# Kernel tuning notes

Hardware: AMD Instinct MI355X
Metric: run time of the kernel (lower is better)

Reference implementation:

```python
import jax, jax.numpy as jnp
import numpy as np


def _pool_matrix(in_size, out_size):
    # Reproduces TF adaptive window bounds: start = int(i*scale), end = ceil((i+1)*scale)
    scale = np.float32(in_size) / np.float32(out_size)
    idx = np.arange(out_size, dtype=np.float32)
    starts = (idx * scale).astype(np.int32)
    ends = np.ceil((idx + 1.0) * scale).astype(np.int32)
    M = np.zeros((out_size, in_size), dtype=np.float32)
    for i in range(out_size):  # loop over small static output size only
        M[i, starts[i]:ends[i]] = 1.0 / float(ends[i] - starts[i])
    return jnp.asarray(M)


def setup_inputs() -> dict:
    key = jax.random.key(0)
    x = jax.random.normal(key, (8, 224, 224, 256), dtype=jnp.float32)
    return {"x": x, "out_h": 7, "out_w": 7}


def reference(x, out_h, out_w):
    # x: [B, H, W, C] NHWC. Adaptive avg pool to [B, out_h, out_w, C].
    # Window means expressed as two small averaging matmuls (exactly equal to
    # the original slice+reduce_mean loops, applied rows-then-columns).
    Mh = _pool_matrix(x.shape[1], out_h)  # [out_h, H]
    Mw = _pool_matrix(x.shape[2], out_w)  # [out_w, W]
    xh = jnp.einsum('oh,bhwc->bowc', Mh, x)      # mean over row windows
    out = jnp.einsum('pw,bowc->bopc', Mw, xh)    # mean over col windows
    return out
```

## Files before the change

kernel.cpp:

```cpp
#include <hip/hip_runtime.h>


constexpr int B  = 8;
constexpr int H  = 224;
constexpr int W  = 224;
constexpr int C  = 256;
constexpr int OH = 7;
constexpr int OW = 7;
constexpr int WIN = 32;
constexpr int CHUNKS = 8;
constexpr int ROWS_PER_CHUNK = WIN / CHUNKS;
constexpr int G  = C / 4;
constexpr int OUT_ELEMS = B * OH * OW * C;
constexpr int NCHUNK_BLOCKS = B * OH * OW * CHUNKS;
constexpr size_t WS_NEEDED = (size_t)NCHUNK_BLOCKS * C * sizeof(float);

__global__ __launch_bounds__(256) void pool_partial_kernel(const float* __restrict__ x,
                                                           float* __restrict__ ws) {
    int bid   = blockIdx.x;
    int chunk = bid & (CHUNKS - 1);
    int t     = bid >> 3;
    int ow    = t % OW; t /= OW;
    int oh    = t % OH; t /= OH;
    int b     = t;

    int tid = threadIdx.x;
    int g   = tid & (G - 1);
    int r   = tid >> 6;

    int row  = oh * WIN + chunk * ROWS_PER_CHUNK + r;
    int col0 = ow * WIN;

    const float4* p = reinterpret_cast<const float4*>(
        x + (((size_t)b * H + row) * W + col0) * C) + g;

    float4 acc = make_float4(0.f, 0.f, 0.f, 0.f);
#pragma unroll
    for (int c = 0; c < WIN; ++c) {
        float4 v = p[(size_t)c * G];
        acc.x += v.x; acc.y += v.y; acc.z += v.z; acc.w += v.w;
    }

    __shared__ float4 lds[ROWS_PER_CHUNK][G];
    lds[r][g] = acc;
    __syncthreads();

    if (r == 0) {
        float4 a0 = lds[0][g];
        float4 a1 = lds[1][g];
        float4 a2 = lds[2][g];
        float4 a3 = lds[3][g];
        float4 s;
        s.x = a0.x + a1.x + a2.x + a3.x;
        s.y = a0.y + a1.y + a2.y + a3.y;
        s.z = a0.z + a1.z + a2.z + a3.z;
        s.w = a0.w + a1.w + a2.w + a3.w;
        reinterpret_cast<float4*>(ws)[(size_t)bid * G + g] = s;
    }
}

__global__ __launch_bounds__(256) void reduce_kernel(const float* __restrict__ ws,
                                                     float* __restrict__ out) {
    int i = blockIdx.x * 256 + threadIdx.x;
    if (i >= OUT_ELEMS) return;
    int o = i >> 8;
    int c = i & (C - 1);
    const float* p = ws + (size_t)(o * CHUNKS) * C + c;
    float s = 0.f;
#pragma unroll
    for (int k = 0; k < CHUNKS; ++k) s += p[(size_t)k * C];
    out[i] = s * (1.0f / (float)(WIN * WIN));
}

__global__ void zero_out_kernel(float* __restrict__ out, int n) {
    int i = blockIdx.x * blockDim.x + threadIdx.x;
    if (i < n) out[i] = 0.0f;
}

__global__ __launch_bounds__(256) void pool_atomic_kernel(const float* __restrict__ x,
                                                          float* __restrict__ out) {
    int bid   = blockIdx.x;
    int chunk = bid & (CHUNKS - 1);
    int t     = bid >> 3;
    int ow    = t % OW; t /= OW;
    int oh    = t % OH; t /= OH;
    int b     = t;

    int tid = threadIdx.x;
    int g   = tid & (G - 1);
    int r   = tid >> 6;

    int row  = oh * WIN + chunk * ROWS_PER_CHUNK + r;
    int col0 = ow * WIN;

    const float4* p = reinterpret_cast<const float4*>(
        x + (((size_t)b * H + row) * W + col0) * C) + g;

    float4 acc = make_float4(0.f, 0.f, 0.f, 0.f);
#pragma unroll
    for (int c = 0; c < WIN; ++c) {
        float4 v = p[(size_t)c * G];
        acc.x += v.x; acc.y += v.y; acc.z += v.z; acc.w += v.w;
    }

    __shared__ float4 lds[ROWS_PER_CHUNK][G];
    lds[r][g] = acc;
    __syncthreads();

    if (r == 0) {
        float4 a0 = lds[0][g];
        float4 a1 = lds[1][g];
        float4 a2 = lds[2][g];
        float4 a3 = lds[3][g];
        const float s = 1.0f / (float)(WIN * WIN);
        float* o = out + (size_t)(bid >> 3) * C + g * 4;
        atomicAdd(o + 0, (a0.x + a1.x + a2.x + a3.x) * s);
        atomicAdd(o + 1, (a0.y + a1.y + a2.y + a3.y) * s);
        atomicAdd(o + 2, (a0.z + a1.z + a2.z + a3.z) * s);
        atomicAdd(o + 3, (a0.w + a1.w + a2.w + a3.w) * s);
    }
}

extern "C" void kernel_launch(void* const* d_in, const int* in_sizes, int n_in,
                              void* d_out, int out_size, void* d_ws, size_t ws_size,
                              hipStream_t stream) {
    const float* x = (const float*)d_in[0];
    float* out = (float*)d_out;

    if (ws_size >= WS_NEEDED) {
        float* ws = (float*)d_ws;
        pool_partial_kernel<<<NCHUNK_BLOCKS, 256, 0, stream>>>(x, ws);
        reduce_kernel<<<(OUT_ELEMS + 255) / 256, 256, 0, stream>>>(ws, out);
    } else {
        zero_out_kernel<<<(OUT_ELEMS + 255) / 256, 256, 0, stream>>>(out, OUT_ELEMS);
        pool_atomic_kernel<<<NCHUNK_BLOCKS, 256, 0, stream>>>(x, out);
    }
}
```

Baseline: 78.25 us.

## Stream whole input rows per block and reduce row partials in second pass

```diff
diff --git a/kernel.cpp b/kernel.cpp
--- a/kernel.cpp
+++ b/kernel.cpp
@@ -8,12 +8,85 @@
 constexpr int OH = 7;
 constexpr int OW = 7;
 constexpr int WIN = 32;
+constexpr int G  = C / 4;
+constexpr int F4_PER_ROW = W * G;
+constexpr int ITERS = F4_PER_ROW / 256;
+constexpr int OUT_ELEMS = B * OH * OW * C;
+constexpr int NROWS = B * H;
+constexpr size_t WS_ROW_NEEDED = (size_t)NROWS * OW * C * sizeof(float);
+
+__global__ __launch_bounds__(256) void row_stream_kernel(const float* __restrict__ x,
+                                                         float* __restrict__ ws) {
+    const int rowid = blockIdx.x;
+    const int tid   = threadIdx.x;
+    const int c4    = tid & (G - 1);
+    const int col0  = tid >> 6;
+
+    const float4* p = reinterpret_cast<const float4*>(x) + (size_t)rowid * F4_PER_ROW + tid;
+
+    float4 acc[OW];
+#pragma unroll
+    for (int o = 0; o < OW; ++o) acc[o] = make_float4(0.f, 0.f, 0.f, 0.f);
+
+#pragma unroll
+    for (int m = 0; m < ITERS; ++m) {
+        float4 v = p[(size_t)m * 256];
+        const int o = m >> 3;
+        acc[o].x += v.x; acc[o].y += v.y; acc[o].z += v.z; acc[o].w += v.w;
+    }
+
+    __shared__ float4 lds[OW][2][G];
+
+    if (col0 >= 2) {
+#pragma unroll
+        for (int o = 0; o < OW; ++o) lds[o][col0 - 2][c4] = acc[o];
+    }
+    __syncthreads();
+    if (col0 < 2) {
+#pragma unroll
+        for (int o = 0; o < OW; ++o) {
+            float4 v = lds[o][col0][c4];
+            acc[o].x += v.x; acc[o].y += v.y; acc[o].z += v.z; acc[o].w += v.w;
+        }
+    }
+    __syncthreads();
+    if (col0 == 1) {
+#pragma unroll
+        for (int o = 0; o < OW; ++o) lds[o][0][c4] = acc[o];
+    }
+    __syncthreads();
+    if (col0 == 0) {
+        float4* wrow = reinterpret_cast<float4*>(ws) + (size_t)rowid * (OW * G);
+#pragma unroll
+        for (int o = 0; o < OW; ++o) {
+            float4 v = lds[o][0][c4];
+            v.x += acc[o].x; v.y += acc[o].y; v.z += acc[o].z; v.w += acc[o].w;
+            wrow[o * G + c4] = v;
+        }
+    }
+}
+
+__global__ __launch_bounds__(256) void row_reduce_kernel(const float* __restrict__ ws,
+                                                         float* __restrict__ out) {
+    int i = blockIdx.x * 256 + threadIdx.x;
+    if (i >= OUT_ELEMS) return;
+    int c  = i & (C - 1);
+    int t  = i >> 8;
+    int ow = t % OW; t /= OW;
+    int oh = t % OH; t /= OH;
+    int b  = t;
+
+    const float* p = ws + (((size_t)(b * H + oh * WIN) * OW) + ow) * C + c;
+    float s = 0.f;
+#pragma unroll
+    for (int r = 0; r < WIN; ++r) s += p[(size_t)r * OW * C];
+    out[i] = s * (1.0f / (float)(WIN * WIN));
+}
+
 constexpr int CHUNKS = 8;
 constexpr int ROWS_PER_CHUNK = WIN / CHUNKS;
-constexpr int G  = C / 4;
-constexpr int OUT_ELEMS = B * OH * OW * C;
 constexpr int NCHUNK_BLOCKS = B * OH * OW * CHUNKS;
-constexpr size_t WS_NEEDED = (size_t)NCHUNK_BLOCKS * C * sizeof(float);
+constexpr size_t WS_CHUNK_NEEDED = (size_t)NCHUNK_BLOCKS * C * sizeof(float);
 
 __global__ __launch_bounds__(256) void pool_partial_kernel(const float* __restrict__ x,
                                                            float* __restrict__ ws) {
@@ -72,67 +145,18 @@
     out[i] = s * (1.0f / (float)(WIN * WIN));
 }
 
-__global__ void zero_out_kernel(float* __restrict__ out, int n) {
-    int i = blockIdx.x * blockDim.x + threadIdx.x;
-    if (i < n) out[i] = 0.0f;
-}
-
-__global__ __launch_bounds__(256) void pool_atomic_kernel(const float* __restrict__ x,
-                                                          float* __restrict__ out) {
-    int bid   = blockIdx.x;
-    int chunk = bid & (CHUNKS - 1);
-    int t     = bid >> 3;
-    int ow    = t % OW; t /= OW;
-    int oh    = t % OH; t /= OH;
-    int b     = t;
-
-    int tid = threadIdx.x;
-    int g   = tid & (G - 1);
-    int r   = tid >> 6;
-
-    int row  = oh * WIN + chunk * ROWS_PER_CHUNK + r;
-    int col0 = ow * WIN;
-
-    const float4* p = reinterpret_cast<const float4*>(
-        x + (((size_t)b * H + row) * W + col0) * C) + g;
-
-    float4 acc = make_float4(0.f, 0.f, 0.f, 0.f);
-#pragma unroll
-    for (int c = 0; c < WIN; ++c) {
-        float4 v = p[(size_t)c * G];
-        acc.x += v.x; acc.y += v.y; acc.z += v.z; acc.w += v.w;
-    }
-
-    __shared__ float4 lds[ROWS_PER_CHUNK][G];
-    lds[r][g] = acc;
-    __syncthreads();
-
-    if (r == 0) {
-        float4 a0 = lds[0][g];
-        float4 a1 = lds[1][g];
-        float4 a2 = lds[2][g];
-        float4 a3 = lds[3][g];
-        const float s = 1.0f / (float)(WIN * WIN);
-        float* o = out + (size_t)(bid >> 3) * C + g * 4;
-        atomicAdd(o + 0, (a0.x + a1.x + a2.x + a3.x) * s);
-        atomicAdd(o + 1, (a0.y + a1.y + a2.y + a3.y) * s);
-        atomicAdd(o + 2, (a0.z + a1.z + a2.z + a3.z) * s);
-        atomicAdd(o + 3, (a0.w + a1.w + a2.w + a3.w) * s);
-    }
-}
-
 extern "C" void kernel_launch(void* const* d_in, const int* in_sizes, int n_in,
                               void* d_out, int out_size, void* d_ws, size_t ws_size,
                               hipStream_t stream) {
     const float* x = (const float*)d_in[0];
     float* out = (float*)d_out;
+    float* ws = (float*)d_ws;
 
-    if (ws_size >= WS_NEEDED) {
-        float* ws = (float*)d_ws;
+    if (ws_size >= WS_ROW_NEEDED) {
+        row_stream_kernel<<<NROWS, 256, 0, stream>>>(x, ws);
+        row_reduce_kernel<<<(OUT_ELEMS + 255) / 256, 256, 0, stream>>>(ws, out);
+    } else {
         pool_partial_kernel<<<NCHUNK_BLOCKS, 256, 0, stream>>>(x, ws);
         reduce_kernel<<<(OUT_ELEMS + 255) / 256, 256, 0, stream>>>(ws, out);
-    } else {
-        zero_out_kernel<<<(OUT_ELEMS + 255) / 256, 256, 0, stream>>>(out, OUT_ELEMS);
-        pool_atomic_kernel<<<NCHUNK_BLOCKS, 256, 0, stream>>>(x, out);
     }
 }
```

Measured after the change: 83.76 us. +7.1%, slower.
